# Kernel tuning notes

Measured on AMD Instinct MI355X. Metric: run time of the kernel, lower is better.

Reference implementation:

```python
import jax, jax.numpy as jnp
import numpy as np

LATENT = 8
HIDDEN = 16
DFEAT = 16
N_LAYERS = 10
G = 64          # num graphs
NPG = 1024      # nodes per graph
E = G * NPG * 16  # edges (avg degree 16)


def setup_inputs() -> dict:
    key = jax.random.key(0)
    ks = jax.random.split(key, 20)
    n = G * NPG
    x = jax.random.normal(ks[0], (n, DFEAT), dtype=jnp.float32)
    eps = jax.random.normal(ks[1], (n, LATENT), dtype=jnp.float32)
    # edges constrained to lie within a graph (block-diagonal structure)
    g = jax.random.randint(ks[2], (E,), 0, G)
    ls = jax.random.randint(ks[3], (E,), 0, NPG)
    ld = jax.random.randint(ks[4], (E,), 0, NPG)
    edge_index = jnp.stack([g * NPG + ls, g * NPG + ld]).astype(jnp.int32)
    s = 0.1
    inp = {
        "x": x, "eps": eps, "edge_index": edge_index, "num_graphs": G,
        # GIN layer 0 MLP (lazy in_channels -> hidden -> hidden)
        "W0a": jax.random.normal(ks[5], (DFEAT, HIDDEN), jnp.float32) * s,
        "b0a": jnp.zeros((HIDDEN,), jnp.float32),
        "W0b": jax.random.normal(ks[6], (HIDDEN, HIDDEN), jnp.float32) * s,
        "b0b": jnp.zeros((HIDDEN,), jnp.float32),
        # GIN layers 1..9 MLPs, stacked
        "Wa": jax.random.normal(ks[7], (N_LAYERS - 1, HIDDEN, HIDDEN), jnp.float32) * s,
        "ba": jnp.zeros((N_LAYERS - 1, HIDDEN), jnp.float32),
        "Wb": jax.random.normal(ks[8], (N_LAYERS - 1, HIDDEN, HIDDEN), jnp.float32) * s,
        "bb": jnp.zeros((N_LAYERS - 1, HIDDEN), jnp.float32),
        # mean / std heads
        "Wm": jax.random.normal(ks[9], (HIDDEN, LATENT), jnp.float32) * s,
        "bm": jnp.zeros((LATENT,), jnp.float32),
        "Ws": jax.random.normal(ks[10], (HIDDEN, LATENT), jnp.float32) * s,
        "bs": jnp.zeros((LATENT,), jnp.float32),
    }
    return inp


def _gin_encode(x, edge_index, W0a, b0a, W0b, b0b, Wa, ba, Wb, bb):
    n = x.shape[0]
    src, dst = edge_index[0], edge_index[1]

    def conv(h, wa, bia, wb, bib):
        # GINConv, eps=0: MLP((1+eps)*h + sum_{j in N(i)} h_j)
        agg = h + jax.ops.segment_sum(h[src], dst, num_segments=n)
        return jax.nn.relu(agg @ wa + bia) @ wb + bib

    h = jax.nn.relu(conv(x, W0a, b0a, W0b, b0b))
    for i in range(Wa.shape[0]):
        h = conv(h, Wa[i], ba[i], Wb[i], bb[i])
        if i < Wa.shape[0] - 1:  # act between layers, not after the last conv
            h = jax.nn.relu(h)
    return h


def _vae_forward(x, eps, edge_index, num_graphs,
                 W0a, b0a, W0b, b0b, Wa, ba, Wb, bb, Wm, bm, Ws, bs):
    n = x.shape[0]
    npg = n // num_graphs
    h = _gin_encode(x, edge_index, W0a, b0a, W0b, b0b, Wa, ba, Wb, bb)
    mu = h @ Wm + bm
    std = jax.nn.softplus(h @ Ws + bs)
    z = mu + std * eps                      # rsample from Normal(mu, std)
    z3 = z.reshape(num_graphs, npg, LATENT)  # per-graph split (equal sizes)
    # inner-product decode per graph, sigmoid act
    adj_pred = jax.nn.sigmoid(jnp.einsum("gnd,gmd->gnm", z3, z3))
    # to_dense_adj on the block-diagonal edge list
    src, dst = edge_index[0], edge_index[1]
    g = src // npg
    dense_adj = jnp.zeros((num_graphs, npg, npg), jnp.float32)
    dense_adj = dense_adj.at[g, src % npg, dst % npg].set(1.0)
    # BCELoss(reduction='sum') with torch's log clamp at -100
    logp = jnp.clip(jnp.log(adj_pred), -100.0)
    log1mp = jnp.clip(jnp.log1p(-adj_pred), -100.0)
    nll = -jnp.sum(dense_adj * logp + (1.0 - dense_adj) * log1mp)
    # KL(N(mu,std) || N(0,1)), summed
    kl = jnp.sum(-jnp.log(std) + 0.5 * (std * std + mu * mu) - 0.5)
    return nll, kl, adj_pred, dense_adj


def reference(x, eps, edge_index, num_graphs,
              W0a, b0a, W0b, b0b, Wa, ba, Wb, bb, Wm, bm, Ws, bs):
    return _vae_forward(x, eps, edge_index, num_graphs,
                        W0a, b0a, W0b, b0b, Wa, ba, Wb, bb, Wm, bm, Ws, bs)
```

## Files before the change

kernel.cpp:

```cpp
#include <hip/hip_runtime.h>
#include <cstddef>

#define G 64
#define NPG 1024
#define NNODES 65536
#define NEDGE 1048576
#define BCAP 48
#define HSTR 20
#define ZTR 1028
#define ADJ_ELEMS 67108864ull
#define BM_WORDS 2097152

typedef float f32x4 __attribute__((ext_vector_type(4)));
typedef float f32x2 __attribute__((ext_vector_type(2)));
typedef unsigned u32x4 __attribute__((ext_vector_type(4)));

__global__ __launch_bounds__(1024) void k_init(int* __restrict__ cnt, float* __restrict__ acc,
                                               unsigned* __restrict__ bm) {
  int i = blockIdx.x * 1024 + threadIdx.x;
  cnt[i] = 0;
  if (i < 2) acc[i] = 0.0f;
  u32x4 z = {0u, 0u, 0u, 0u};
  u32x4* b4 = (u32x4*)bm;
  for (int k = i; k < BM_WORDS / 4; k += 65536) b4[k] = z;
}

__global__ __launch_bounds__(256) void k_build(const int* __restrict__ ei,
                                               int* __restrict__ cnt,
                                               unsigned short* __restrict__ colb,
                                               unsigned* __restrict__ bm) {
  int stride = gridDim.x * blockDim.x;
  for (int e = blockIdx.x * blockDim.x + threadIdx.x; e < NEDGE; e += stride) {
    int src = ei[e], dst = ei[NEDGE + e];
    int p = atomicAdd(&cnt[dst], 1);
    if (p < BCAP) colb[(size_t)dst * BCAP + p] = (unsigned short)(src & (NPG - 1));
    int gg = src >> 10, ls = src & (NPG - 1), ld = dst & (NPG - 1);
    atomicOr(&bm[gg * 32768 + ls * 32 + (ld >> 5)], 1u << (ld & 31));
  }
}

__global__ __launch_bounds__(1024) void k_gin(
    const float* __restrict__ x, const float* __restrict__ eps,
    const int* __restrict__ cnt, const unsigned short* __restrict__ colb,
    const float* __restrict__ W0a, const float* __restrict__ b0a,
    const float* __restrict__ W0b, const float* __restrict__ b0b,
    const float* __restrict__ Wa, const float* __restrict__ ba,
    const float* __restrict__ Wb, const float* __restrict__ bb,
    const float* __restrict__ Wm, const float* __restrict__ bm_,
    const float* __restrict__ Ws, const float* __restrict__ bs,
    const unsigned* __restrict__ ebm,
    float* __restrict__ zbuf, float* __restrict__ acc, float* __restrict__ out) {
  __shared__ float hbuf[NPG * HSTR];
  __shared__ float red[16];

  if (blockIdx.x >= G) {
    f32x4* dz = (f32x4*)(out + 2 + ADJ_ELEMS);
    size_t i = (size_t)(blockIdx.x - G) * 1024 + threadIdx.x;
    size_t stride = (size_t)(gridDim.x - G) * 1024;
    for (; i < ADJ_ELEMS / 4; i += stride) {
      unsigned w = ebm[i >> 3];
      int sh = ((int)i & 7) << 2;
      f32x4 v;
      v.x = ((w >> (sh + 0)) & 1) ? 1.f : 0.f;
      v.y = ((w >> (sh + 1)) & 1) ? 1.f : 0.f;
      v.z = ((w >> (sh + 2)) & 1) ? 1.f : 0.f;
      v.w = ((w >> (sh + 3)) & 1) ? 1.f : 0.f;
      __builtin_nontemporal_store(v, &dz[i]);
    }
    return;
  }

  const int g = blockIdx.x;
  const int tid = threadIdx.x;
  const int dv0 = cnt[g * NPG + tid];
  const int dv = (dv0 < BCAP) ? dv0 : BCAP;
  const unsigned short* cl = colb + (size_t)(g * NPG + tid) * BCAP;

  {
    const float4* xg = (const float4*)(x + (size_t)g * (NPG * 16));
    for (int idx = tid; idx < NPG * 4; idx += 1024) {
      float4 v = xg[idx];
      *(float4*)(hbuf + (idx >> 2) * HSTR + (idx & 3) * 4) = v;
    }
  }
  __syncthreads();

  for (int l = 0; l < 10; ++l) {
    const float* Aw = (l == 0) ? W0a : Wa + (l - 1) * 256;
    const float* Ab = (l == 0) ? b0a : ba + (l - 1) * 16;
    const float* Bw = (l == 0) ? W0b : Wb + (l - 1) * 256;
    const float* Bb = (l == 0) ? b0b : bb + (l - 1) * 16;

    float4 a0 = *(const float4*)(hbuf + tid * HSTR + 0);
    float4 a1 = *(const float4*)(hbuf + tid * HSTR + 4);
    float4 a2 = *(const float4*)(hbuf + tid * HSTR + 8);
    float4 a3 = *(const float4*)(hbuf + tid * HSTR + 12);
    for (int k = 0; k < dv; ++k) {
      int ls = cl[k];
      const float* hp = hbuf + ls * HSTR;
      float4 v0 = *(const float4*)(hp + 0);
      float4 v1 = *(const float4*)(hp + 4);
      float4 v2 = *(const float4*)(hp + 8);
      float4 v3 = *(const float4*)(hp + 12);
      a0.x += v0.x; a0.y += v0.y; a0.z += v0.z; a0.w += v0.w;
      a1.x += v1.x; a1.y += v1.y; a1.z += v1.z; a1.w += v1.w;
      a2.x += v2.x; a2.y += v2.y; a2.z += v2.z; a2.w += v2.w;
      a3.x += v3.x; a3.y += v3.y; a3.z += v3.z; a3.w += v3.w;
    }
    float aa[16] = {a0.x, a0.y, a0.z, a0.w, a1.x, a1.y, a1.z, a1.w,
                    a2.x, a2.y, a2.z, a2.w, a3.x, a3.y, a3.z, a3.w};

    float u[16], v[16];
    #pragma unroll
    for (int j = 0; j < 16; ++j) u[j] = Ab[j];
    #pragma unroll
    for (int i = 0; i < 16; ++i) {
      float ai = aa[i];
      #pragma unroll
      for (int j = 0; j < 16; ++j) u[j] += ai * Aw[i * 16 + j];
    }
    #pragma unroll
    for (int j = 0; j < 16; ++j) u[j] = fmaxf(u[j], 0.f);
    #pragma unroll
    for (int j = 0; j < 16; ++j) v[j] = Bb[j];
    #pragma unroll
    for (int i = 0; i < 16; ++i) {
      float ui = u[i];
      #pragma unroll
      for (int j = 0; j < 16; ++j) v[j] += ui * Bw[i * 16 + j];
    }
    const bool rl = (l != 9);
    __syncthreads();
    #pragma unroll
    for (int j4 = 0; j4 < 4; ++j4) {
      float4 w;
      w.x = rl ? fmaxf(v[j4 * 4 + 0], 0.f) : v[j4 * 4 + 0];
      w.y = rl ? fmaxf(v[j4 * 4 + 1], 0.f) : v[j4 * 4 + 1];
      w.z = rl ? fmaxf(v[j4 * 4 + 2], 0.f) : v[j4 * 4 + 2];
      w.w = rl ? fmaxf(v[j4 * 4 + 3], 0.f) : v[j4 * 4 + 3];
      *(float4*)(hbuf + tid * HSTR + j4 * 4) = w;
    }
    __syncthreads();
  }

  float hv[16];
  #pragma unroll
  for (int i = 0; i < 16; ++i) hv[i] = hbuf[tid * HSTR + i];

  float mu[8], st[8];
  #pragma unroll
  for (int m = 0; m < 8; ++m) { mu[m] = bm_[m]; st[m] = bs[m]; }
  #pragma unroll
  for (int i = 0; i < 16; ++i) {
    float hi = hv[i];
    #pragma unroll
    for (int m = 0; m < 8; ++m) { mu[m] += hi * Wm[i * 8 + m]; st[m] += hi * Ws[i * 8 + m]; }
  }
  #pragma unroll
  for (int m = 0; m < 8; ++m) {
    float s = st[m];
    st[m] = fmaxf(s, 0.f) + log1pf(__expf(-fabsf(s)));
  }
  int gid = g * NPG + tid;
  float4 e0 = *(const float4*)(eps + (size_t)gid * 8);
  float4 e1 = *(const float4*)(eps + (size_t)gid * 8 + 4);
  float ev[8] = {e0.x, e0.y, e0.z, e0.w, e1.x, e1.y, e1.z, e1.w};
  float zv[8];
  float klp = 0.f;
  #pragma unroll
  for (int m = 0; m < 8; ++m) {
    zv[m] = mu[m] + st[m] * ev[m];
    klp += -__logf(st[m]) + 0.5f * (st[m] * st[m] + mu[m] * mu[m]) - 0.5f;
  }
  *(float4*)(zbuf + (size_t)gid * 8) = make_float4(zv[0], zv[1], zv[2], zv[3]);
  *(float4*)(zbuf + (size_t)gid * 8 + 4) = make_float4(zv[4], zv[5], zv[6], zv[7]);

  for (int o = 32; o > 0; o >>= 1) klp += __shfl_down(klp, o, 64);
  if ((tid & 63) == 0) red[tid >> 6] = klp;
  __syncthreads();
  if (tid == 0) {
    float s = 0.f;
    for (int i = 0; i < 16; ++i) s += red[i];
    atomicAdd(&acc[1], s);
  }
}

__device__ __forceinline__ float elem_p(float sv, int bit, float& accl) {
  float t = __expf(-sv);
  float p = __builtin_amdgcn_rcpf(1.f + t);
  float lp, lm;
  if (t > 3.0e38f)             { lp = -100.f; lm = 0.f; }
  else if (t < 5.9604645e-08f) { lp = 0.f;    lm = -100.f; }
  else { float q = __logf(1.f + t); lp = -q; lm = -sv - q; }
  accl += bit ? lp : lm;
  return p;
}

__global__ __launch_bounds__(256) void k_adj(const float* __restrict__ zbuf,
                                             const unsigned* __restrict__ ebm,
                                             float* __restrict__ out,
                                             float* __restrict__ acc) {
  __shared__ float zt[8 * ZTR];
  __shared__ float red[4];
  const int tid = threadIdx.x;
  const int g = blockIdx.x >> 6;
  const int i0 = (blockIdx.x & 63) << 4;

  {
    const float4* zg = (const float4*)(zbuf + (size_t)g * (NPG * 8));
    #pragma unroll
    for (int it = 0; it < 8; ++it) {
      int idx = tid + it * 256;
      float4 v = zg[idx];
      int j = idx >> 1, db = (idx & 1) << 2;
      zt[(db + 0) * ZTR + j] = v.x;
      zt[(db + 1) * ZTR + j] = v.y;
      zt[(db + 2) * ZTR + j] = v.z;
      zt[(db + 3) * ZTR + j] = v.w;
    }
  }
  __syncthreads();

  const int w = tid >> 6;
  const int l = tid & 63;
  float accl = 0.f;

  for (int ir = 0; ir < 4; ++ir) {
    const int i = i0 + (w << 2) + ir;
    float zi[8];
    #pragma unroll
    for (int d = 0; d < 8; ++d) zi[d] = zt[d * ZTR + i];
    const unsigned* bmrow = ebm + g * 32768 + i * 32;
    float* orow = out + 2 + (size_t)g * (NPG * NPG) + (size_t)i * NPG;
    #pragma unroll
    for (int jp = 0; jp < 4; ++jp) {
      const int j0 = (l << 2) + (jp << 8);
      float s0 = 0.f, s1 = 0.f, s2 = 0.f, s3 = 0.f;
      #pragma unroll
      for (int d = 0; d < 8; ++d) {
        float4 zr = *(const float4*)(zt + d * ZTR + j0);
        float zd = zi[d];
        s0 += zd * zr.x; s1 += zd * zr.y; s2 += zd * zr.z; s3 += zd * zr.w;
      }
      unsigned bits = (bmrow[j0 >> 5] >> (j0 & 31)) & 15u;
      float p0 = elem_p(s0, bits & 1, accl);
      float p1 = elem_p(s1, (bits >> 1) & 1, accl);
      float p2 = elem_p(s2, (bits >> 2) & 1, accl);
      float p3 = elem_p(s3, (bits >> 3) & 1, accl);
      f32x2 v0 = {p0, p1}, v1 = {p2, p3};
      f32x2* dp = (f32x2*)(orow + j0);
      __builtin_nontemporal_store(v0, &dp[0]);
      __builtin_nontemporal_store(v1, &dp[1]);
    }
  }

  for (int o = 32; o > 0; o >>= 1) accl += __shfl_down(accl, o, 64);
  if (l == 0) red[w] = accl;
  __syncthreads();
  if (tid == 0) atomicAdd(&acc[0], red[0] + red[1] + red[2] + red[3]);
}

__global__ void k_fin(const float* __restrict__ acc, float* __restrict__ out) {
  if (threadIdx.x == 0 && blockIdx.x == 0) {
    out[0] = -acc[0];
    out[1] = acc[1];
  }
}

extern "C" void kernel_launch(void* const* d_in, const int* in_sizes, int n_in,
                              void* d_out, int out_size, void* d_ws, size_t ws_size,
                              hipStream_t stream) {
  const float* x   = (const float*)d_in[0];
  const float* eps = (const float*)d_in[1];
  const int*   ei  = (const int*)d_in[2];
  const float* W0a = (const float*)d_in[4];
  const float* b0a = (const float*)d_in[5];
  const float* W0b = (const float*)d_in[6];
  const float* b0b = (const float*)d_in[7];
  const float* Wa  = (const float*)d_in[8];
  const float* ba  = (const float*)d_in[9];
  const float* Wb  = (const float*)d_in[10];
  const float* bb  = (const float*)d_in[11];
  const float* Wm  = (const float*)d_in[12];
  const float* bm  = (const float*)d_in[13];
  const float* Ws  = (const float*)d_in[14];
  const float* bs  = (const float*)d_in[15];
  float* out = (float*)d_out;

  int* cnt             = (int*)d_ws;
  unsigned short* colb = (unsigned short*)(cnt + NNODES);
  float* zbuf          = (float*)(colb + (size_t)NNODES * BCAP);
  unsigned* ebm        = (unsigned*)(zbuf + (size_t)NNODES * 8);
  float* acc           = (float*)(ebm + BM_WORDS);

  k_init<<<64, 1024, 0, stream>>>(cnt, acc, ebm);
  k_build<<<1024, 256, 0, stream>>>(ei, cnt, colb, ebm);
  k_gin<<<256, 1024, 0, stream>>>(x, eps, cnt, colb,
                                  W0a, b0a, W0b, b0b, Wa, ba, Wb, bb,
                                  Wm, bm, Ws, bs, ebm, zbuf, acc, out);
  k_adj<<<4096, 256, 0, stream>>>(zbuf, ebm, out, acc);
  k_fin<<<1, 64, 0, stream>>>(acc, out);
}
```

Baseline: 351.1 us.

## Stage per-node neighbor lists in LDS and vectorize edge loads in build

Each GIN block now copies the first 32 neighbor indices of every node into a transposed shared-memory table once. All ten layers then read neighbor indices from LDS instead of reloading them from global memory; neighbors beyond 32 still fall back to the global list. The build kernel also loads four edges per thread with int4 reads instead of using a grid-stride loop. That change assumes the launch covers exactly NEDGE/4 threads. The extra 64KB of LDS raises per-block shared-memory use, and an empty leftover loop remains.

```diff
diff --git a/kernel.cpp b/kernel.cpp
--- a/kernel.cpp
+++ b/kernel.cpp
@@ -6,6 +6,7 @@
 #define NNODES 65536
 #define NEDGE 1048576
 #define BCAP 48
+#define LCAP 32
 #define HSTR 20
 #define ZTR 1028
 #define ADJ_ELEMS 67108864ull
@@ -29,9 +30,16 @@
                                                int* __restrict__ cnt,
                                                unsigned short* __restrict__ colb,
                                                unsigned* __restrict__ bm) {
-  int stride = gridDim.x * blockDim.x;
-  for (int e = blockIdx.x * blockDim.x + threadIdx.x; e < NEDGE; e += stride) {
-    int src = ei[e], dst = ei[NEDGE + e];
+  int t = blockIdx.x * 256 + threadIdx.x;
+  const int4* sp = (const int4*)ei;
+  const int4* dp = (const int4*)(ei + NEDGE);
+  int4 s4 = sp[t];
+  int4 d4 = dp[t];
+  int ss[4] = {s4.x, s4.y, s4.z, s4.w};
+  int dd[4] = {d4.x, d4.y, d4.z, d4.w};
+  #pragma unroll
+  for (int q = 0; q < 4; ++q) {
+    int src = ss[q], dst = dd[q];
     int p = atomicAdd(&cnt[dst], 1);
     if (p < BCAP) colb[(size_t)dst * BCAP + p] = (unsigned short)(src & (NPG - 1));
     int gg = src >> 10, ls = src & (NPG - 1), ld = dst & (NPG - 1);
@@ -51,6 +59,7 @@
     const unsigned* __restrict__ ebm,
     float* __restrict__ zbuf, float* __restrict__ acc, float* __restrict__ out) {
   __shared__ float hbuf[NPG * HSTR];
+  __shared__ unsigned short colc[NPG * LCAP];
   __shared__ float red[16];
 
   if (blockIdx.x >= G) {
@@ -74,7 +83,28 @@
   const int tid = threadIdx.x;
   const int dv0 = cnt[g * NPG + tid];
   const int dv = (dv0 < BCAP) ? dv0 : BCAP;
+  const int dvl = (dv < LCAP) ? dv : LCAP;
   const unsigned short* cl = colb + (size_t)(g * NPG + tid) * BCAP;
+
+  {
+    const uint4* rowp = (const uint4*)(colb + (size_t)(g * NPG + tid) * BCAP);
+    #pragma unroll
+    for (int q = 0; q < 2; ++q) {
+    }
+    #pragma unroll
+    for (int q = 0; q < 4; ++q) {
+      uint4 w4 = rowp[q];
+      unsigned ws0 = w4.x, ws1 = w4.y, ws2 = w4.z, ws3 = w4.w;
+      colc[(q * 8 + 0) * NPG + tid] = (unsigned short)(ws0 & 0xffff);
+      colc[(q * 8 + 1) * NPG + tid] = (unsigned short)(ws0 >> 16);
+      colc[(q * 8 + 2) * NPG + tid] = (unsigned short)(ws1 & 0xffff);
+      colc[(q * 8 + 3) * NPG + tid] = (unsigned short)(ws1 >> 16);
+      colc[(q * 8 + 4) * NPG + tid] = (unsigned short)(ws2 & 0xffff);
+      colc[(q * 8 + 5) * NPG + tid] = (unsigned short)(ws2 >> 16);
+      colc[(q * 8 + 6) * NPG + tid] = (unsigned short)(ws3 & 0xffff);
+      colc[(q * 8 + 7) * NPG + tid] = (unsigned short)(ws3 >> 16);
+    }
+  }
 
   {
     const float4* xg = (const float4*)(x + (size_t)g * (NPG * 16));
@@ -95,7 +125,19 @@
     float4 a1 = *(const float4*)(hbuf + tid * HSTR + 4);
     float4 a2 = *(const float4*)(hbuf + tid * HSTR + 8);
     float4 a3 = *(const float4*)(hbuf + tid * HSTR + 12);
-    for (int k = 0; k < dv; ++k) {
+    for (int k = 0; k < dvl; ++k) {
+      int ls = colc[k * NPG + tid];
+      const float* hp = hbuf + ls * HSTR;
+      float4 v0 = *(const float4*)(hp + 0);
+      float4 v1 = *(const float4*)(hp + 4);
+      float4 v2 = *(const float4*)(hp + 8);
+      float4 v3 = *(const float4*)(hp + 12);
+      a0.x += v0.x; a0.y += v0.y; a0.z += v0.z; a0.w += v0.w;
+      a1.x += v1.x; a1.y += v1.y; a1.z += v1.z; a1.w += v1.w;
+      a2.x += v2.x; a2.y += v2.y; a2.z += v2.z; a2.w += v2.w;
+      a3.x += v3.x; a3.y += v3.y; a3.z += v3.z; a3.w += v3.w;
+    }
+    for (int k = LCAP; k < dv; ++k) {
       int ls = cl[k];
       const float* hp = hbuf + ls * HSTR;
       float4 v0 = *(const float4*)(hp + 0);
```

Result: faster. 330.2 us (-6.0%).
